# Kernel tuning notes

Measured on AMD Instinct MI355X. Metric: run time of the kernel, lower is better.

The kernel has to match this reference:

```python
import jax, jax.numpy as jnp
import numpy as np

N, M, NCAPS, NHID, ROUTIT = 50000, 16, 8, 16, 6
D = NCAPS * NHID  # 128


def _normalize(x, axis):
    # torch fn.normalize: x / max(||x||, eps)
    return x / jnp.maximum(jnp.linalg.norm(x, axis=axis, keepdims=True), 1e-12)


def _routing(x, nb, k, dd, max_iter, fc_w=None, fc_b=None):
    # x: [n, d], nb: [n*m] int indices into rows of x (n == zero pad row)
    if fc_w is not None:
        x = jax.nn.relu(x @ fc_w.T + fc_b)
    n = x.shape[0]
    d = k * dd
    m = nb.shape[0] // n
    xn = _normalize(x.reshape(n, k, dd), 2)          # [n,k,dd]
    zsrc = jnp.concatenate([xn.reshape(n, d), jnp.zeros((1, d), x.dtype)], axis=0)
    z = zsrc[nb].reshape(n, m, k, dd)                # gathered neighbors
    u = xn
    for it in range(max_iter):
        p = jax.nn.softmax(jnp.einsum('nmkd,nkd->nmk', z, u), axis=2)
        u = jnp.einsum('nmkd,nmk->nkd', z, p) + xn
        if it < max_iter - 1:
            u = _normalize(u, 2)
    return u.reshape(n, d)


def setup_inputs() -> dict:
    key = jax.random.key(0)
    k1, k2, k3 = jax.random.split(key, 3)
    x = jax.random.normal(k1, (N, D), dtype=jnp.float32)
    nb = jax.random.randint(k2, (N * M,), 0, N)
    fc1_w = jax.random.normal(k3, (D, D), dtype=jnp.float32) * (1.0 / np.sqrt(D))
    fc1_b = jnp.zeros((D,), dtype=jnp.float32)
    return {"x": x, "nb": nb, "fc1_w": fc1_w, "fc1_b": fc1_b}


def reference(x, nb, fc1_w, fc1_b):
    nb = nb.reshape(-1)
    # layer 0: inp_caps=None -> no fc; dropout is identity in eval mode
    h = jax.nn.relu(_routing(x, nb, NCAPS, NHID, ROUTIT))
    # layer 1: fc Linear(D, D) then relu inside routing
    h = jax.nn.relu(_routing(h, nb, NCAPS, NHID, ROUTIT, fc1_w, fc1_b))
    return h
```

## Files before the change

### kernel.cpp

```cpp
#include <hip/hip_runtime.h>
#include <math.h>

#define N_NODES 50000
#define M_NB 16
#define K_CAPS 8
#define DD 16
#define D_DIM 128
#define ROUTIT 6

template <int CTRL>
__device__ __forceinline__ float dpp_add(float x) {
    int t = __builtin_amdgcn_update_dpp(0, __float_as_int(x), CTRL, 0xF, 0xF, true);
    return x + __int_as_float(t);
}

__device__ __forceinline__ float xor8_add(float x) {
    float d;
    asm("s_nop 1\n\t"
        "v_add_f32_dpp %0, %1, %1 row_ror:8 row_mask:0xf bank_mask:0xf"
        : "=v"(d) : "v"(x));
    return d;
}

__device__ __forceinline__ float xor16_add(float x) {
#if __has_builtin(__builtin_amdgcn_permlane16_swap)
    unsigned xi = __float_as_uint(x);
    auto r = __builtin_amdgcn_permlane16_swap(xi, xi, false, false);
    return __uint_as_float(r[0]) + __uint_as_float(r[1]);
#else
    return x + __int_as_float(__builtin_amdgcn_ds_swizzle(__float_as_int(x), 0x401F));
#endif
}

__device__ __forceinline__ float xor32_add(float x) {
#if __has_builtin(__builtin_amdgcn_permlane32_swap)
    unsigned xi = __float_as_uint(x);
    auto r = __builtin_amdgcn_permlane32_swap(xi, xi, false, false);
    return __uint_as_float(r[0]) + __uint_as_float(r[1]);
#else
    return x + __shfl_xor(x, 32);
#endif
}

__device__ __forceinline__ float fast_rcp(float x) {
#if __has_builtin(__builtin_amdgcn_rcpf)
    return __builtin_amdgcn_rcpf(x);
#else
    return 1.0f / x;
#endif
}

__device__ __forceinline__ float fast_rsq(float x) {
#if __has_builtin(__builtin_amdgcn_rsqf)
    return __builtin_amdgcn_rsqf(x);
#else
    return 1.0f / sqrtf(x);
#endif
}

__device__ __forceinline__ float fast_exp2(float x) {
#if __has_builtin(__builtin_amdgcn_exp2f)
    return __builtin_amdgcn_exp2f(x);
#else
    return __expf(x * 0.6931471805599453f);
#endif
}

__device__ __forceinline__ float2 pk_fma(float2 a, float2 b, float2 c) {
    float2 d;
    asm("v_pk_fma_f32 %0, %1, %2, %3" : "=v"(d) : "v"(a), "v"(b), "v"(c));
    return d;
}

#define BFLY16(CTRLSTR)                                                        \
    asm ("s_nop 1\n\t"                                                         \
         "v_add_f32_dpp %0, %0, %0 "   CTRLSTR "\n\t"                          \
         "v_add_f32_dpp %1, %1, %1 "   CTRLSTR "\n\t"                          \
         "v_add_f32_dpp %2, %2, %2 "   CTRLSTR "\n\t"                          \
         "v_add_f32_dpp %3, %3, %3 "   CTRLSTR "\n\t"                          \
         "v_add_f32_dpp %4, %4, %4 "   CTRLSTR "\n\t"                          \
         "v_add_f32_dpp %5, %5, %5 "   CTRLSTR "\n\t"                          \
         "v_add_f32_dpp %6, %6, %6 "   CTRLSTR "\n\t"                          \
         "v_add_f32_dpp %7, %7, %7 "   CTRLSTR "\n\t"                          \
         "v_add_f32_dpp %8, %8, %8 "   CTRLSTR "\n\t"                          \
         "v_add_f32_dpp %9, %9, %9 "   CTRLSTR "\n\t"                          \
         "v_add_f32_dpp %10, %10, %10 " CTRLSTR "\n\t"                         \
         "v_add_f32_dpp %11, %11, %11 " CTRLSTR "\n\t"                         \
         "v_add_f32_dpp %12, %12, %12 " CTRLSTR "\n\t"                         \
         "v_add_f32_dpp %13, %13, %13 " CTRLSTR "\n\t"                         \
         "v_add_f32_dpp %14, %14, %14 " CTRLSTR "\n\t"                         \
         "v_add_f32_dpp %15, %15, %15 " CTRLSTR                                \
         : "+v"(u[0].x), "+v"(u[0].y), "+v"(u[1].x), "+v"(u[1].y),             \
           "+v"(u[2].x), "+v"(u[2].y), "+v"(u[3].x), "+v"(u[3].y),             \
           "+v"(u[4].x), "+v"(u[4].y), "+v"(u[5].x), "+v"(u[5].y),             \
           "+v"(u[6].x), "+v"(u[6].y), "+v"(u[7].x), "+v"(u[7].y))

__global__ void normalize_kernel(const float* __restrict__ x,
                                 float* __restrict__ xn) {
    int tid = blockIdx.x * blockDim.x + threadIdx.x;
    if (tid >= N_NODES * K_CAPS) return;
    const float4* p = reinterpret_cast<const float4*>(x + (size_t)tid * DD);
    float4 a0 = p[0], a1 = p[1], a2 = p[2], a3 = p[3];
    float s = a0.x*a0.x + a0.y*a0.y + a0.z*a0.z + a0.w*a0.w
            + a1.x*a1.x + a1.y*a1.y + a1.z*a1.z + a1.w*a1.w
            + a2.x*a2.x + a2.y*a2.y + a2.z*a2.z + a2.w*a2.w
            + a3.x*a3.x + a3.y*a3.y + a3.z*a3.z + a3.w*a3.w;
    float inv = 1.0f / fmaxf(sqrtf(s), 1e-12f);
    float4* q = reinterpret_cast<float4*>(xn + (size_t)tid * DD);
    a0.x *= inv; a0.y *= inv; a0.z *= inv; a0.w *= inv;
    a1.x *= inv; a1.y *= inv; a1.z *= inv; a1.w *= inv;
    a2.x *= inv; a2.y *= inv; a2.z *= inv; a2.w *= inv;
    a3.x *= inv; a3.y *= inv; a3.z *= inv; a3.w *= inv;
    q[0] = a0; q[1] = a1; q[2] = a2; q[3] = a3;
}

__global__ __launch_bounds__(256)
void routing_kernel(const float* __restrict__ xn,
                    const int* __restrict__ nb,
                    float* __restrict__ out) {
    const int wave = threadIdx.x >> 6;
    const int lane = threadIdx.x & 63;
    const int node = blockIdx.x * 4 + wave;
    const int mh = lane & 7;
    const int k  = lane >> 3;

    const int idx0 = nb[node * M_NB + mh];
    const int idx1 = nb[node * M_NB + mh + 8];
    const float* zr0 = xn + (size_t)idx0 * D_DIM + k * DD;
    const float* zr1 = xn + (size_t)idx1 * D_DIM + k * DD;

    float2 z0[8], z1[8];
#pragma unroll
    for (int j = 0; j < 4; ++j) {
        float4 a = *reinterpret_cast<const float4*>(zr0 + j * 4);
        z0[2*j]     = make_float2(a.x, a.y);
        z0[2*j + 1] = make_float2(a.z, a.w);
        float4 b = *reinterpret_cast<const float4*>(zr1 + j * 4);
        z1[2*j]     = make_float2(b.x, b.y);
        z1[2*j + 1] = make_float2(b.z, b.w);
    }

    const float* xrow = xn + (size_t)node * D_DIM + k * DD;
    float2 u[8], xs[8];
#pragma unroll
    for (int j = 0; j < 4; ++j) {
        float4 v = *reinterpret_cast<const float4*>(xrow + j * 4);
        u[2*j]     = make_float2(v.x, v.y);
        u[2*j + 1] = make_float2(v.z, v.w);
        xs[2*j]     = make_float2(v.x * 0.125f, v.y * 0.125f);
        xs[2*j + 1] = make_float2(v.z * 0.125f, v.w * 0.125f);
    }

    const float LOG2E = 1.4426950408889634f;
    const float2 zero2 = make_float2(0.f, 0.f);
    float s2 = LOG2E;

#pragma unroll
    for (int it = 0; it < ROUTIT; ++it) {
        float2 a0 = pk_fma(z0[0], u[0], zero2);
        float2 a1 = pk_fma(z0[1], u[1], zero2);
        a0 = pk_fma(z0[2], u[2], a0);
        a1 = pk_fma(z0[3], u[3], a1);
        a0 = pk_fma(z0[4], u[4], a0);
        a1 = pk_fma(z0[5], u[5], a1);
        a0 = pk_fma(z0[6], u[6], a0);
        a1 = pk_fma(z0[7], u[7], a1);
        float2 b0 = pk_fma(z1[0], u[0], zero2);
        float2 b1 = pk_fma(z1[1], u[1], zero2);
        b0 = pk_fma(z1[2], u[2], b0);
        b1 = pk_fma(z1[3], u[3], b1);
        b0 = pk_fma(z1[4], u[4], b0);
        b1 = pk_fma(z1[5], u[5], b1);
        b0 = pk_fma(z1[6], u[6], b0);
        b1 = pk_fma(z1[7], u[7], b1);
        float l0 = (a0.x + a0.y) + (a1.x + a1.y);
        float l1 = (b0.x + b0.y) + (b1.x + b1.y);

        float e0 = fast_exp2(l0 * s2);
        float e1 = fast_exp2(l1 * s2);
        float t0 = xor8_add(e0);  float t1 = xor8_add(e1);
        t0 = xor16_add(t0);       t1 = xor16_add(t1);
        t0 = xor32_add(t0);       t1 = xor32_add(t1);
        float p0 = e0 * fast_rcp(t0);
        float p1 = e1 * fast_rcp(t1);

        float2 p0b = make_float2(p0, p0);
        float2 p1b = make_float2(p1, p1);
#pragma unroll
        for (int j = 0; j < 8; ++j)
            u[j] = pk_fma(z1[j], p1b, pk_fma(z0[j], p0b, xs[j]));

        BFLY16("quad_perm:[1,0,3,2] row_mask:0xf bank_mask:0xf");
        BFLY16("quad_perm:[2,3,0,1] row_mask:0xf bank_mask:0xf");
        BFLY16("row_half_mirror row_mask:0xf bank_mask:0xf");

        if (it < ROUTIT - 1) {
            float2 q0 = pk_fma(u[0], u[0], zero2);
            float2 q1 = pk_fma(u[1], u[1], zero2);
            q0 = pk_fma(u[2], u[2], q0);
            q1 = pk_fma(u[3], u[3], q1);
            q0 = pk_fma(u[4], u[4], q0);
            q1 = pk_fma(u[5], u[5], q1);
            q0 = pk_fma(u[6], u[6], q0);
            q1 = pk_fma(u[7], u[7], q1);
            float nrm = (q0.x + q0.y) + (q1.x + q1.y);
            s2 = fast_rsq(fmaxf(nrm, 1e-24f)) * LOG2E;
        }
    }

#pragma unroll
    for (int j = 0; j < 8; ++j) {
        u[j].x = fmaxf(u[j].x, 0.f);
        u[j].y = fmaxf(u[j].y, 0.f);
    }
#pragma unroll
    for (int j = 0; j < 4; ++j) {
        if (mh == j) {
            float4 v = make_float4(u[2*j].x, u[2*j].y, u[2*j+1].x, u[2*j+1].y);
            *reinterpret_cast<float4*>(out + (size_t)node * D_DIM + k * DD + j * 4) = v;
        }
    }
}

__global__ __launch_bounds__(256, 2)
void fc_norm_kernel(const float* __restrict__ h,
                    const float* __restrict__ W,
                    const float* __restrict__ b,
                    float* __restrict__ xnout) {
    __shared__ float4 Wt4[32 * 129];
    __shared__ float4 hrow4[8 * 32];

    const float4* W4 = reinterpret_cast<const float4*>(W);
    for (int t = threadIdx.x; t < 128 * 32; t += 256) {
        Wt4[(t & 31) * 129 + (t >> 5)] = W4[t];
    }
    __syncthreads();

    const int col = threadIdx.x & 127;
    const int rr  = threadIdx.x >> 7;
    const float bias = b[col];

    for (int row0 = blockIdx.x * 8; row0 < N_NODES; row0 += gridDim.x * 8) {
        __syncthreads();
        {
            int t = threadIdx.x;
            hrow4[t] = *reinterpret_cast<const float4*>(
                h + (size_t)(row0 + (t >> 5)) * D_DIM + (t & 31) * 4);
        }
        __syncthreads();

        float acc0 = bias, acc1 = bias, acc2 = bias, acc3 = bias;
#pragma unroll
        for (int k4 = 0; k4 < 32; ++k4) {
            float4 w4 = Wt4[k4 * 129 + col];
            float4 h0 = hrow4[(rr * 4 + 0) * 32 + k4];
            float4 h1 = hrow4[(rr * 4 + 1) * 32 + k4];
            float4 h2 = hrow4[(rr * 4 + 2) * 32 + k4];
            float4 h3 = hrow4[(rr * 4 + 3) * 32 + k4];
            acc0 = fmaf(w4.x, h0.x, acc0); acc0 = fmaf(w4.y, h0.y, acc0);
            acc0 = fmaf(w4.z, h0.z, acc0); acc0 = fmaf(w4.w, h0.w, acc0);
            acc1 = fmaf(w4.x, h1.x, acc1); acc1 = fmaf(w4.y, h1.y, acc1);
            acc1 = fmaf(w4.z, h1.z, acc1); acc1 = fmaf(w4.w, h1.w, acc1);
            acc2 = fmaf(w4.x, h2.x, acc2); acc2 = fmaf(w4.y, h2.y, acc2);
            acc2 = fmaf(w4.z, h2.z, acc2); acc2 = fmaf(w4.w, h2.w, acc2);
            acc3 = fmaf(w4.x, h3.x, acc3); acc3 = fmaf(w4.y, h3.y, acc3);
            acc3 = fmaf(w4.z, h3.z, acc3); acc3 = fmaf(w4.w, h3.w, acc3);
        }

        float a[4] = {fmaxf(acc0, 0.f), fmaxf(acc1, 0.f),
                      fmaxf(acc2, 0.f), fmaxf(acc3, 0.f)};
#pragma unroll
        for (int j = 0; j < 4; ++j) {
            float s = a[j] * a[j];
            s = dpp_add<0xB1>(s);
            s = dpp_add<0x4E>(s);
            s = dpp_add<0x141>(s);
            s = dpp_add<0x140>(s);
            float inv = fast_rsq(fmaxf(s, 1e-24f));
            xnout[(size_t)(row0 + rr * 4 + j) * D_DIM + col] = a[j] * inv;
        }
    }
}

extern "C" void kernel_launch(void* const* d_in, const int* in_sizes, int n_in,
                              void* d_out, int out_size, void* d_ws, size_t ws_size,
                              hipStream_t stream) {
    const float* x  = (const float*)d_in[0];
    const int*   nb = (const int*)d_in[1];
    const float* W  = (const float*)d_in[2];
    const float* bb = (const float*)d_in[3];
    float* out = (float*)d_out;

    float* xnbuf = (float*)d_ws;
    float* h0    = xnbuf + (size_t)N_NODES * D_DIM;

    normalize_kernel<<<(N_NODES * K_CAPS + 255) / 256, 256, 0, stream>>>(x, xnbuf);
    routing_kernel<<<N_NODES / 4, 256, 0, stream>>>(xnbuf, nb, h0);
    fc_norm_kernel<<<1024, 256, 0, stream>>>(h0, W, bb, xnbuf);
    routing_kernel<<<N_NODES / 4, 256, 0, stream>>>(xnbuf, nb, out);
}
```

Baseline: 218.3 us.

## Store normalized capsule features in bf16 to halve gather traffic

Result: faster. 205.1 us (-6.0%).

```diff
diff --git a/kernel.cpp b/kernel.cpp
--- a/kernel.cpp
+++ b/kernel.cpp
@@ -70,6 +70,23 @@
     float2 d;
     asm("v_pk_fma_f32 %0, %1, %2, %3" : "=v"(d) : "v"(a), "v"(b), "v"(c));
     return d;
+}
+
+__device__ __forceinline__ float2 bf2(unsigned w) {
+    return make_float2(__uint_as_float(w << 16),
+                       __uint_as_float(w & 0xFFFF0000u));
+}
+
+__device__ __forceinline__ unsigned cvt_pk_bf16(float lo, float hi) {
+    unsigned r;
+    asm("v_cvt_pk_bf16_f32 %0, %1, %2" : "=v"(r) : "v"(lo), "v"(hi));
+    return r;
+}
+
+__device__ __forceinline__ unsigned short f2bf(float v) {
+    unsigned u = __float_as_uint(v);
+    u = (u + 0x7FFFu + ((u >> 16) & 1u)) >> 16;
+    return (unsigned short)u;
 }
 
 #define BFLY16(CTRLSTR)                                                        \
@@ -96,7 +113,7 @@
            "+v"(u[6].x), "+v"(u[6].y), "+v"(u[7].x), "+v"(u[7].y))
 
 __global__ void normalize_kernel(const float* __restrict__ x,
-                                 float* __restrict__ xn) {
+                                 unsigned short* __restrict__ xnb) {
     int tid = blockIdx.x * blockDim.x + threadIdx.x;
     if (tid >= N_NODES * K_CAPS) return;
     const float4* p = reinterpret_cast<const float4*>(x + (size_t)tid * DD);
@@ -106,16 +123,21 @@
             + a2.x*a2.x + a2.y*a2.y + a2.z*a2.z + a2.w*a2.w
             + a3.x*a3.x + a3.y*a3.y + a3.z*a3.z + a3.w*a3.w;
     float inv = 1.0f / fmaxf(sqrtf(s), 1e-12f);
-    float4* q = reinterpret_cast<float4*>(xn + (size_t)tid * DD);
     a0.x *= inv; a0.y *= inv; a0.z *= inv; a0.w *= inv;
     a1.x *= inv; a1.y *= inv; a1.z *= inv; a1.w *= inv;
     a2.x *= inv; a2.y *= inv; a2.z *= inv; a2.w *= inv;
     a3.x *= inv; a3.y *= inv; a3.z *= inv; a3.w *= inv;
-    q[0] = a0; q[1] = a1; q[2] = a2; q[3] = a3;
+    uint4 w0, w1;
+    w0.x = cvt_pk_bf16(a0.x, a0.y); w0.y = cvt_pk_bf16(a0.z, a0.w);
+    w0.z = cvt_pk_bf16(a1.x, a1.y); w0.w = cvt_pk_bf16(a1.z, a1.w);
+    w1.x = cvt_pk_bf16(a2.x, a2.y); w1.y = cvt_pk_bf16(a2.z, a2.w);
+    w1.z = cvt_pk_bf16(a3.x, a3.y); w1.w = cvt_pk_bf16(a3.z, a3.w);
+    uint4* q = reinterpret_cast<uint4*>(xnb + (size_t)tid * DD);
+    q[0] = w0; q[1] = w1;
 }
 
 __global__ __launch_bounds__(256)
-void routing_kernel(const float* __restrict__ xn,
+void routing_kernel(const unsigned short* __restrict__ xnb,
                     const int* __restrict__ nb,
                     float* __restrict__ out) {
     const int wave = threadIdx.x >> 6;
@@ -126,30 +148,24 @@
 
     const int idx0 = nb[node * M_NB + mh];
     const int idx1 = nb[node * M_NB + mh + 8];
-    const float* zr0 = xn + (size_t)idx0 * D_DIM + k * DD;
-    const float* zr1 = xn + (size_t)idx1 * D_DIM + k * DD;
-
-    float2 z0[8], z1[8];
-#pragma unroll
-    for (int j = 0; j < 4; ++j) {
-        float4 a = *reinterpret_cast<const float4*>(zr0 + j * 4);
-        z0[2*j]     = make_float2(a.x, a.y);
-        z0[2*j + 1] = make_float2(a.z, a.w);
-        float4 b = *reinterpret_cast<const float4*>(zr1 + j * 4);
-        z1[2*j]     = make_float2(b.x, b.y);
-        z1[2*j + 1] = make_float2(b.z, b.w);
-    }
-
-    const float* xrow = xn + (size_t)node * D_DIM + k * DD;
-    float2 u[8], xs[8];
-#pragma unroll
-    for (int j = 0; j < 4; ++j) {
-        float4 v = *reinterpret_cast<const float4*>(xrow + j * 4);
-        u[2*j]     = make_float2(v.x, v.y);
-        u[2*j + 1] = make_float2(v.z, v.w);
-        xs[2*j]     = make_float2(v.x * 0.125f, v.y * 0.125f);
-        xs[2*j + 1] = make_float2(v.z * 0.125f, v.w * 0.125f);
-    }
+    const uint4* zp0 = reinterpret_cast<const uint4*>(xnb + (size_t)idx0 * D_DIM + k * DD);
+    const uint4* zp1 = reinterpret_cast<const uint4*>(xnb + (size_t)idx1 * D_DIM + k * DD);
+    uint4 A0 = zp0[0], A1 = zp0[1];
+    uint4 B0 = zp1[0], B1 = zp1[1];
+
+    const uint4* xp = reinterpret_cast<const uint4*>(xnb + (size_t)node * D_DIM + k * DD);
+    uint4 X0 = xp[0], X1 = xp[1];
+
+    float2 z0[8], z1[8], u[8], xs[8];
+    z0[0] = bf2(A0.x); z0[1] = bf2(A0.y); z0[2] = bf2(A0.z); z0[3] = bf2(A0.w);
+    z0[4] = bf2(A1.x); z0[5] = bf2(A1.y); z0[6] = bf2(A1.z); z0[7] = bf2(A1.w);
+    z1[0] = bf2(B0.x); z1[1] = bf2(B0.y); z1[2] = bf2(B0.z); z1[3] = bf2(B0.w);
+    z1[4] = bf2(B1.x); z1[5] = bf2(B1.y); z1[6] = bf2(B1.z); z1[7] = bf2(B1.w);
+    u[0] = bf2(X0.x); u[1] = bf2(X0.y); u[2] = bf2(X0.z); u[3] = bf2(X0.w);
+    u[4] = bf2(X1.x); u[5] = bf2(X1.y); u[6] = bf2(X1.z); u[7] = bf2(X1.w);
+#pragma unroll
+    for (int j = 0; j < 8; ++j)
+        xs[j] = make_float2(u[j].x * 0.125f, u[j].y * 0.125f);
 
     const float LOG2E = 1.4426950408889634f;
     const float2 zero2 = make_float2(0.f, 0.f);
@@ -226,7 +242,7 @@
 void fc_norm_kernel(const float* __restrict__ h,
                     const float* __restrict__ W,
                     const float* __restrict__ b,
-                    float* __restrict__ xnout) {
+                    unsigned short* __restrict__ xnbout) {
     __shared__ float4 Wt4[32 * 129];
     __shared__ float4 hrow4[8 * 32];
 
@@ -277,7 +293,7 @@
             s = dpp_add<0x141>(s);
             s = dpp_add<0x140>(s);
             float inv = fast_rsq(fmaxf(s, 1e-24f));
-            xnout[(size_t)(row0 + rr * 4 + j) * D_DIM + col] = a[j] * inv;
+            xnbout[(size_t)(row0 + rr * 4 + j) * D_DIM + col] = f2bf(a[j] * inv);
         }
     }
 }
@@ -291,11 +307,11 @@
     const float* bb = (const float*)d_in[3];
     float* out = (float*)d_out;
 
-    float* xnbuf = (float*)d_ws;
-    float* h0    = xnbuf + (size_t)N_NODES * D_DIM;
-
-    normalize_kernel<<<(N_NODES * K_CAPS + 255) / 256, 256, 0, stream>>>(x, xnbuf);
-    routing_kernel<<<N_NODES / 4, 256, 0, stream>>>(xnbuf, nb, h0);
-    fc_norm_kernel<<<1024, 256, 0, stream>>>(h0, W, bb, xnbuf);
-    routing_kernel<<<N_NODES / 4, 256, 0, stream>>>(xnbuf, nb, out);
-}
+    unsigned short* xnb = (unsigned short*)d_ws;
+    float* h0 = (float*)((char*)d_ws + (size_t)N_NODES * D_DIM * 2);
+
+    normalize_kernel<<<(N_NODES * K_CAPS + 255) / 256, 256, 0, stream>>>(x, xnb);
+    routing_kernel<<<N_NODES / 4, 256, 0, stream>>>(xnb, nb, h0);
+    fc_norm_kernel<<<1024, 256, 0, stream>>>(h0, W, bb, xnb);
+    routing_kernel<<<N_NODES / 4, 256, 0, stream>>>(xnb, nb, out);
+}
```
